# Performance work log

Hardware: AMD Instinct MI355X
Metric: run time of the kernel (lower is better)

Reference implementation:

```python
import jax, jax.numpy as jnp
from jax import lax
import numpy as np

D_MODEL, N_STATES, N_GROUPS, K_CONV = 1024, 16, 8, 4
BATCH, LENGTH = 2, 2048


def setup_inputs() -> dict:
    key = jax.random.key(0)
    ks = jax.random.split(key, 8)
    x = jax.random.normal(ks[0], (BATCH, LENGTH, D_MODEL), dtype=jnp.float32)
    in_proj_w = jax.random.normal(ks[1], (2 * D_MODEL, D_MODEL), dtype=jnp.float32) * 0.02
    in_proj_b = jnp.zeros((2 * D_MODEL,), dtype=jnp.float32)
    delta_proj_w = jax.random.uniform(ks[2], (D_MODEL, D_MODEL), dtype=jnp.float32, minval=0.001, maxval=0.1)
    a_log = jnp.log(jnp.tile(jnp.arange(1, N_STATES + 1, dtype=jnp.float32), (D_MODEL, 1)))
    b_proj_w = jax.random.normal(ks[3], (N_GROUPS * N_STATES, D_MODEL), dtype=jnp.float32) * 1e-4
    b_proj_b = jnp.zeros((N_GROUPS * N_STATES,), dtype=jnp.float32)
    c_param = jax.random.normal(ks[4], (D_MODEL, N_STATES), dtype=jnp.float32) * 0.02
    # depthwise conv (groups = d_model): kernel [D, 1, K]
    conv_w = jax.random.normal(ks[5], (D_MODEL, 1, K_CONV), dtype=jnp.float32) * (1.0 / np.sqrt(K_CONV))
    conv_b = jnp.zeros((D_MODEL,), dtype=jnp.float32)
    return {"x": x, "in_proj_w": in_proj_w, "in_proj_b": in_proj_b,
            "delta_proj_w": delta_proj_w, "a_log": a_log,
            "b_proj_w": b_proj_w, "b_proj_b": b_proj_b, "c_param": c_param,
            "conv_w": conv_w, "conv_b": conv_b}


def _causal_conv(u, conv_w, conv_b):
    # u: [B, L, D] -> depthwise causal conv along L
    D = u.shape[-1]
    K = conv_w.shape[-1]
    uc = jnp.transpose(u, (0, 2, 1))  # [B, D, L]
    uc = lax.conv_general_dilated(uc, conv_w, window_strides=(1,),
                                  padding=[(K - 1, 0)], feature_group_count=D,
                                  dimension_numbers=("NCH", "OIH", "NCH"))
    uc = uc + conv_b[None, :, None]
    return jnp.transpose(uc, (0, 2, 1))  # [B, L, D]


def _selective_scan(delta, A, Bmat, c_param, u):
    # delta,u: [B,L,D]; A: [D,N]; Bmat: [B,L,G,N]; c_param: [D,N]
    Bsz, L, D = delta.shape
    N = A.shape[1]
    G = Bmat.shape[2]
    Bexp = jnp.repeat(Bmat, D // G, axis=2)            # [B,L,D,N]
    dA = jnp.exp(delta[..., None] * A)                  # [B,L,D,N]
    dBu = (delta * u)[..., None] * Bexp                 # [B,L,D,N]

    def step(h, xs):
        da, dbu = xs
        h = da * h + dbu                                # [B,D,N]
        y = jnp.einsum("bdn,dn->bd", h, c_param)
        return h, y

    h0 = jnp.zeros((Bsz, D, N), dtype=delta.dtype)
    _, ys = lax.scan(step, h0, (jnp.moveaxis(dA, 1, 0), jnp.moveaxis(dBu, 1, 0)))
    return jnp.moveaxis(ys, 0, 1)                       # [B,L,D]


def reference(x, in_proj_w, in_proj_b, delta_proj_w, a_log, b_proj_w, b_proj_b, c_param, conv_w, conv_b):
    Bsz, L, _ = x.shape
    N = a_log.shape[1]
    G = b_proj_w.shape[0] // N
    xp = x @ in_proj_w.T + in_proj_b                    # [B,L,2D]
    u, v = jnp.split(xp, 2, axis=-1)
    delta = jax.nn.softplus(u @ delta_proj_w.T)         # [B,L,D]
    A = -jnp.exp(a_log)                                 # [D,N]
    Bmat = (u @ b_proj_w.T + b_proj_b).reshape(Bsz, L, G, N)
    u_conv = jax.nn.silu(_causal_conv(u, conv_w, conv_b))
    y = _selective_scan(delta, A, Bmat, c_param, u_conv)
    return y * jax.nn.silu(v)
```

## Files before the change

### kernel.cpp

```cpp
#include <hip/hip_runtime.h>
#include <math.h>

#define LTOT 2048
#define MROWS 4096
#define CHK 64
#define NCH (LTOT / CHK)
#define SPAD 20

typedef short bf16x8 __attribute__((ext_vector_type(8)));
typedef float f32x4  __attribute__((ext_vector_type(4)));

__device__ __forceinline__ unsigned short bf16_rne(float f) {
  unsigned u = __float_as_uint(f);
  u += 0x7FFF + ((u >> 16) & 1);
  return (unsigned short)(u >> 16);
}
__device__ __forceinline__ float bf16_to_f(unsigned short h) {
  return __uint_as_float(((unsigned)h) << 16);
}
__device__ __forceinline__ float softplus_f(float x) {
  return (x > 15.f) ? x : log1pf(expf(x));
}
__device__ __forceinline__ float silu_f(float x) {
  return x / (1.f + expf(-x));
}

__global__ __launch_bounds__(256) void k_prep(
    const float* __restrict__ x, const float* __restrict__ w1,
    const float* __restrict__ dw, const float* __restrict__ bw,
    const float* __restrict__ b1, const float* __restrict__ bb,
    unsigned short* __restrict__ xh, unsigned short* __restrict__ wfh,
    unsigned short* __restrict__ wdbAh, unsigned short* __restrict__ wdbAl,
    unsigned short* __restrict__ w1th, unsigned short* __restrict__ w1tl,
    float* __restrict__ bfull) {
  __shared__ float ts[64][65];
  const int blk = blockIdx.x;
  const int t = threadIdx.x;

  if (blk < 6144) {
    const float* src; unsigned short* h; int i;
    if (blk < 4096) { src = x;  h = xh;  i = blk * 256 + t; }
    else            { src = w1; h = wfh; i = (blk - 4096) * 256 + t; }
    const float4 v = ((const float4*)src)[i];
    ushort4 hh;
    hh.x = bf16_rne(v.x); hh.y = bf16_rne(v.y);
    hh.z = bf16_rne(v.z); hh.w = bf16_rne(v.w);
    ((ushort4*)h)[i] = hh;
  } else if (blk < 7296) {
    const float* src; unsigned short *h, *l; int i;
    if (blk < 7168) { src = dw; h = wdbAh; l = wdbAl; i = (blk - 6144) * 256 + t; }
    else            { src = bw; h = wdbAh + (size_t)1024*1024; l = wdbAl + (size_t)1024*1024;
                      i = (blk - 7168) * 256 + t; }
    const float4 v = ((const float4*)src)[i];
    ushort4 hh, ll;
    hh.x = bf16_rne(v.x); ll.x = bf16_rne(v.x - bf16_to_f(hh.x));
    hh.y = bf16_rne(v.y); ll.y = bf16_rne(v.y - bf16_to_f(hh.y));
    hh.z = bf16_rne(v.z); ll.z = bf16_rne(v.z - bf16_to_f(hh.z));
    hh.w = bf16_rne(v.w); ll.w = bf16_rne(v.w - bf16_to_f(hh.w));
    ((ushort4*)h)[i] = hh;
    ((ushort4*)l)[i] = ll;
  } else if (blk < 7552) {
    const int s = blk - 7296;
    const int k0 = (s & 15) * 64, j0 = (s >> 4) * 64;
    const int r = t >> 4, c4 = (t & 15) * 4;
    #pragma unroll
    for (int p = 0; p < 4; ++p) {
      const int row = p * 16 + r;
      const float4 v = *(const float4*)&w1[(size_t)(j0 + row) * 1024 + k0 + c4];
      ts[row][c4] = v.x; ts[row][c4+1] = v.y; ts[row][c4+2] = v.z; ts[row][c4+3] = v.w;
    }
    __syncthreads();
    #pragma unroll
    for (int p = 0; p < 4; ++p) {
      const int rk = p * 16 + r;
      ushort4 hh, ll;
      float f;
      f = ts[c4+0][rk]; hh.x = bf16_rne(f); ll.x = bf16_rne(f - bf16_to_f(hh.x));
      f = ts[c4+1][rk]; hh.y = bf16_rne(f); ll.y = bf16_rne(f - bf16_to_f(hh.y));
      f = ts[c4+2][rk]; hh.z = bf16_rne(f); ll.z = bf16_rne(f - bf16_to_f(hh.z));
      f = ts[c4+3][rk]; hh.w = bf16_rne(f); ll.w = bf16_rne(f - bf16_to_f(hh.w));
      *(ushort4*)&w1th[(size_t)(k0 + rk) * 1024 + j0 + c4] = hh;
      *(ushort4*)&w1tl[(size_t)(k0 + rk) * 1024 + j0 + c4] = ll;
    }
  } else {
    const int j = (blk - 7552) * 16 + (t >> 4);
    const int lane16 = t & 15;
    const float* W = (j < 1024) ? (dw + (size_t)j * 1024) : (bw + (size_t)(j - 1024) * 1024);
    float s = 0.f;
    for (int i = 0; i < 64; ++i) {
      const int k = lane16 + i * 16;
      s = fmaf(b1[k], W[k], s);
    }
    s += __shfl_xor(s, 8, 16);
    s += __shfl_xor(s, 4, 16);
    s += __shfl_xor(s, 2, 16);
    s += __shfl_xor(s, 1, 16);
    if (lane16 == 0) bfull[j] = s + ((j >= 1024) ? bb[j - 1024] : 0.f);
  }
}

__global__ __launch_bounds__(256) void k_wcomp2(
    const unsigned short* __restrict__ Ah_g, const unsigned short* __restrict__ Al_g,
    const unsigned short* __restrict__ Bh_g, const unsigned short* __restrict__ Bl_g,
    unsigned short* __restrict__ outh) {
  __shared__ __align__(16) unsigned short LAh[128*32];
  __shared__ __align__(16) unsigned short LAl[128*32];
  __shared__ __align__(16) unsigned short LBh[128*32];
  __shared__ __align__(16) unsigned short LBl[128*32];
  const int t = threadIdx.x;
  const int wave = t >> 6, lane = t & 63;
  const int m0 = blockIdx.y * 128;
  const int n0 = blockIdx.x * 128;
  const int wr = wave >> 1, wc = wave & 1;
  const int ln = lane & 15, kq = lane >> 4;
  const int srow = lane >> 2, scol = (lane & 3) * 8;

  f32x4 acc[4][4];
  #pragma unroll
  for (int i = 0; i < 4; ++i)
    #pragma unroll
    for (int j = 0; j < 4; ++j) acc[i][j] = (f32x4){0.f, 0.f, 0.f, 0.f};

  const unsigned short* pAh = Ah_g + (size_t)m0 * 1024;
  const unsigned short* pAl = Al_g + (size_t)m0 * 1024;
  const unsigned short* pBh = Bh_g + (size_t)n0 * 1024;
  const unsigned short* pBl = Bl_g + (size_t)n0 * 1024;

  auto stage = [&](const unsigned short* g, unsigned short* lds, int k0) {
    #pragma unroll
    for (int r = 0; r < 2; ++r) {
      const unsigned short* gp = g + (size_t)(r * 64 + wave * 16 + srow) * 1024 + k0 + scol;
      unsigned short* lp = lds + (r * 64 + wave * 16) * 32;
      __builtin_amdgcn_global_load_lds((const __attribute__((address_space(1))) void*)gp,
                                       (__attribute__((address_space(3))) void*)lp, 16, 0, 0);
    }
  };

  for (int k0 = 0; k0 < 1024; k0 += 32) {
    __syncthreads();
    stage(pAh, LAh, k0);
    stage(pAl, LAl, k0);
    stage(pBh, LBh, k0);
    stage(pBl, LBl, k0);
    __syncthreads();
    bf16x8 ah[4], al[4], bh[4], bl[4];
    #pragma unroll
    for (int i = 0; i < 4; ++i) {
      const int ar = (wr * 64 + i * 16 + ln) * 32 + kq * 8;
      const int br = (wc * 64 + i * 16 + ln) * 32 + kq * 8;
      ah[i] = *(const bf16x8*)&LAh[ar];
      al[i] = *(const bf16x8*)&LAl[ar];
      bh[i] = *(const bf16x8*)&LBh[br];
      bl[i] = *(const bf16x8*)&LBl[br];
    }
    #pragma unroll
    for (int i = 0; i < 4; ++i)
      #pragma unroll
      for (int j = 0; j < 4; ++j) {
        acc[i][j] = __builtin_amdgcn_mfma_f32_16x16x32_bf16(ah[i], bh[j], acc[i][j], 0, 0, 0);
        acc[i][j] = __builtin_amdgcn_mfma_f32_16x16x32_bf16(ah[i], bl[j], acc[i][j], 0, 0, 0);
        acc[i][j] = __builtin_amdgcn_mfma_f32_16x16x32_bf16(al[i], bh[j], acc[i][j], 0, 0, 0);
      }
  }

  const int rbase = (blockIdx.y < 8) ? 2176 : 1024;
  #pragma unroll
  for (int nj = 0; nj < 4; ++nj) {
    const int kcol = n0 + wc * 64 + nj * 16 + ln;
    #pragma unroll
    for (int mi = 0; mi < 4; ++mi) {
      const int i = m0 + wr * 64 + mi * 16 + kq * 4;
      #pragma unroll
      for (int j = 0; j < 4; ++j)
        outh[(size_t)(rbase + i + j) * 1024 + kcol] = bf16_rne(acc[mi][nj][j]);
    }
  }
}

__global__ __launch_bounds__(256) void k_mm_u(
    const unsigned short* __restrict__ xh, const unsigned short* __restrict__ wfh,
    const float* __restrict__ b1, const float* __restrict__ bfull,
    float* __restrict__ u_, float* __restrict__ v_,
    float* __restrict__ delta, float* __restrict__ Bm) {
  __shared__ __align__(16) unsigned short LAh[128*64];
  __shared__ __align__(16) unsigned short LBh[128*64];
  const int t = threadIdx.x;
  const int wave = t >> 6, lane = t & 63;
  const int flat = blockIdx.x;
  const int wg = (flat & 7) * 100 + (flat >> 3);
  const int tn = wg % 25;
  const int m0 = (wg / 25) * 128;
  const int wr = wave >> 1, wc = wave & 1;
  const int ln = lane & 15, kq = lane >> 4;
  const int srow = lane >> 3;
  const int scb  = ((lane & 7) ^ (lane >> 3)) * 8;

  f32x4 acc[4][4];
  #pragma unroll
  for (int i = 0; i < 4; ++i)
    #pragma unroll
    for (int j = 0; j < 4; ++j) acc[i][j] = (f32x4){0.f, 0.f, 0.f, 0.f};

  const unsigned short* pAh = xh + (size_t)m0 * 1024;
  const unsigned short* pBh = wfh + (size_t)(tn * 128) * 1024;

  auto stage = [&](const unsigned short* g, unsigned short* lds, int k0) {
    #pragma unroll
    for (int r = 0; r < 4; ++r) {
      const int rowb = wave * 32 + r * 8;
      const unsigned short* gp = g + (size_t)(rowb + srow) * 1024 + k0 + scb;
      unsigned short* lp = lds + rowb * 64;
      __builtin_amdgcn_global_load_lds((const __attribute__((address_space(1))) void*)gp,
                                       (__attribute__((address_space(3))) void*)lp, 16, 0, 0);
    }
  };

  for (int k0 = 0; k0 < 1024; k0 += 64) {
    __syncthreads();
    stage(pAh, LAh, k0);
    stage(pBh, LBh, k0);
    __syncthreads();
    #pragma unroll
    for (int kh = 0; kh < 2; ++kh) {
      bf16x8 ah[4], bh[4];
      #pragma unroll
      for (int i = 0; i < 4; ++i) {
        const int arow = wr * 64 + i * 16 + ln;
        const int brow = wc * 64 + i * 16 + ln;
        const int ablk = ((kh * 4 + kq) ^ (arow & 7)) * 8;
        const int bblk = ((kh * 4 + kq) ^ (brow & 7)) * 8;
        ah[i] = *(const bf16x8*)&LAh[arow * 64 + ablk];
        bh[i] = *(const bf16x8*)&LBh[brow * 64 + bblk];
      }
      #pragma unroll
      for (int i = 0; i < 4; ++i)
        #pragma unroll
        for (int j = 0; j < 4; ++j)
          acc[i][j] = __builtin_amdgcn_mfma_f32_16x16x32_bf16(ah[i], bh[j], acc[i][j], 0, 0, 0);
    }
  }

  #pragma unroll
  for (int nj = 0; nj < 4; ++nj) {
    const int colg = tn * 128 + wc * 64 + nj * 16 + ln;
    float bv;
    if (colg < 2048)      bv = b1[colg];
    else if (colg < 2176) bv = bfull[1024 + colg - 2048];
    else                  bv = bfull[colg - 2176];
    #pragma unroll
    for (int mi = 0; mi < 4; ++mi) {
      const int row = m0 + wr * 64 + mi * 16 + kq * 4;
      #pragma unroll
      for (int j = 0; j < 4; ++j) {
        const float val = acc[mi][nj][j] + bv;
        if (tn < 8)        u_[(size_t)(row + j) * 1024 + colg] = val;
        else if (tn < 16)  v_[(size_t)(row + j) * 1024 + colg - 1024] = val;
        else if (tn == 16) Bm[(size_t)(row + j) * 128 + colg - 2048] = val;
        else               delta[(size_t)(row + j) * 1024 + colg - 2176] = softplus_f(val);
      }
    }
  }
}

__global__ __launch_bounds__(256) void k_scanA(
    const float* __restrict__ delta, const float* __restrict__ u_,
    const float* __restrict__ Bm, const float* __restrict__ a_log,
    const float* __restrict__ cw, const float* __restrict__ cb,
    float* __restrict__ hend, float* __restrict__ Pp)
{
  __shared__ float sru[68][SPAD];
  __shared__ float sd[CHK][SPAD];
  __shared__ float sb[CHK][SPAD];
  __shared__ float suc[CHK][SPAD];
  const int t = threadIdx.x;
  const int bid = blockIdx.x;
  const int dblk = bid & 63;
  const int ch   = (bid >> 6) & (NCH - 1);
  const int b    = bid >> 11;
  const int d0 = dblk * 16;
  const int g  = dblk >> 3;
  const int l0 = ch * CHK;
  const size_t mb = (size_t)b * LTOT;

  {
    const int lrow = t >> 2;
    const int lc4  = (t & 3) * 4;
    const size_t r = mb + l0 + lrow;
    float4 rd = *(const float4*)&delta[r*1024 + d0 + lc4];
    float4 rb = *(const float4*)&Bm[r*128 + g*16 + lc4];
    *(float4*)&sd[lrow][lc4] = rd;
    *(float4*)&sb[lrow][lc4] = rb;
    const int sl = l0 + lrow - 4;
    float4 ru = (sl >= 0) ? *(const float4*)&u_[(mb + sl)*1024 + d0 + lc4]
                          : (float4){0.f, 0.f, 0.f, 0.f};
    *(float4*)&sru[lrow][lc4] = ru;
    if (t < 16) {
      const int rr2 = 64 + (t >> 2);
      const int sl2 = l0 + rr2 - 4;
      float4 r2 = *(const float4*)&u_[(mb + sl2)*1024 + d0 + (t & 3) * 4];
      *(float4*)&sru[rr2][(t & 3) * 4] = r2;
    }
  }
  __syncthreads();
  {
    const int c = t & 15;
    const int rb4 = (t >> 4) * 4;
    const float4 cwf = *(const float4*)&cw[(d0 + c) * 4];
    const float cbf = cb[d0 + c];
    #pragma unroll
    for (int q = 0; q < 4; ++q) {
      const int l = rb4 + q;
      float a = cbf;
      a = fmaf(sru[l+1][c], cwf.x, a);
      a = fmaf(sru[l+2][c], cwf.y, a);
      a = fmaf(sru[l+3][c], cwf.z, a);
      a = fmaf(sru[l+4][c], cwf.w, a);
      suc[l][c] = silu_f(a);
    }
  }
  __syncthreads();

  const int gi = t >> 4;
  const int n  = t & 15;
  const int d  = d0 + gi;
  const float A2 = -expf(a_log[d*16 + n]) * 1.4426950408889634f;

  float h = 0.f, P = 1.f;
  #pragma unroll 8
  for (int l = 0; l < CHK; ++l) {
    const float dv = sd[l][gi];
    const float uv = suc[l][gi];
    const float bv = sb[l][n];
    const float da = exp2f(dv * A2);
    P *= da;
    h = fmaf(da, h, dv * uv * bv);
  }
  const size_t idx = ((size_t)(b*NCH + ch) * 1024 + d) * 16 + n;
  hend[idx] = h;
  Pp[idx]   = P;
}

__global__ void k_scanB(float* hP, const float* __restrict__ Pp)
{
  const int t = blockIdx.x * 256 + threadIdx.x;
  const int b  = t >> 14;
  const int dn = t & 16383;
  float H = 0.f;
  for (int ch = 0; ch < NCH; ++ch) {
    const size_t idx = ((size_t)(b*NCH + ch) << 14) + dn;
    const float he = hP[idx];
    const float P  = Pp[idx];
    hP[idx] = H;
    H = fmaf(P, H, he);
  }
}

__global__ __launch_bounds__(256) void k_scanC(
    const float* __restrict__ v_, const float* __restrict__ delta,
    const float* __restrict__ u_, const float* __restrict__ Bm,
    const float* __restrict__ a_log, const float* __restrict__ cp,
    const float* __restrict__ cw, const float* __restrict__ cb,
    const float* __restrict__ Hstart, float* __restrict__ out)
{
  __shared__ float sru[68][SPAD];
  __shared__ float sd[CHK][SPAD];
  __shared__ float sb[CHK][SPAD];
  __shared__ float suc[CHK][SPAD];
  __shared__ float sv[CHK][SPAD];
  __shared__ float sy[CHK][SPAD];
  const int t = threadIdx.x;
  const int bid = blockIdx.x;
  const int dblk = bid & 63;
  const int ch   = (bid >> 6) & (NCH - 1);
  const int b    = bid >> 11;
  const int d0 = dblk * 16;
  const int g  = dblk >> 3;
  const int l0 = ch * CHK;
  const size_t mb = (size_t)b * LTOT;

  {
    const int lrow = t >> 2;
    const int lc4  = (t & 3) * 4;
    const size_t r = mb + l0 + lrow;
    float4 rd = *(const float4*)&delta[r*1024 + d0 + lc4];
    float4 rb = *(const float4*)&Bm[r*128 + g*16 + lc4];
    float4 rv = *(const float4*)&v_[r*1024 + d0 + lc4];
    *(float4*)&sd[lrow][lc4] = rd;
    *(float4*)&sb[lrow][lc4] = rb;
    *(float4*)&sv[lrow][lc4] = rv;
    const int sl = l0 + lrow - 4;
    float4 ru = (sl >= 0) ? *(const float4*)&u_[(mb + sl)*1024 + d0 + lc4]
                          : (float4){0.f, 0.f, 0.f, 0.f};
    *(float4*)&sru[lrow][lc4] = ru;
    if (t < 16) {
      const int rr2 = 64 + (t >> 2);
      const int sl2 = l0 + rr2 - 4;
      float4 r2 = *(const float4*)&u_[(mb + sl2)*1024 + d0 + (t & 3) * 4];
      *(float4*)&sru[rr2][(t & 3) * 4] = r2;
    }
  }
  __syncthreads();
  {
    const int c = t & 15;
    const int rb4 = (t >> 4) * 4;
    const float4 cwf = *(const float4*)&cw[(d0 + c) * 4];
    const float cbf = cb[d0 + c];
    #pragma unroll
    for (int q = 0; q < 4; ++q) {
      const int l = rb4 + q;
      float a = cbf;
      a = fmaf(sru[l+1][c], cwf.x, a);
      a = fmaf(sru[l+2][c], cwf.y, a);
      a = fmaf(sru[l+3][c], cwf.z, a);
      a = fmaf(sru[l+4][c], cwf.w, a);
      suc[l][c] = silu_f(a);
    }
  }
  __syncthreads();

  const int gi = t >> 4;
  const int n  = t & 15;
  const int d  = d0 + gi;
  const float A2 = -expf(a_log[d*16 + n]) * 1.4426950408889634f;
  const float cc = cp[d*16 + n];
  float h = Hstart[((size_t)(b*NCH + ch) * 1024 + d) * 16 + n];

  #pragma unroll
  for (int l16 = 0; l16 < CHK; l16 += 16) {
    float p[16];
    #pragma unroll
    for (int j = 0; j < 16; ++j) {
      const int l = l16 + j;
      const float dv = sd[l][gi];
      const float uv = suc[l][gi];
      const float bv = sb[l][n];
      const float da = exp2f(dv * A2);
      h = fmaf(da, h, dv * uv * bv);
      p[j] = h * cc;
    }
    float q8[8];
    #pragma unroll
    for (int j = 0; j < 8; ++j) {
      const float send = (n & 8) ? p[j]     : p[j + 8];
      const float keep = (n & 8) ? p[j + 8] : p[j];
      q8[j] = keep + __shfl_xor(send, 8, 16);
    }
    float q4[4];
    #pragma unroll
    for (int j = 0; j < 4; ++j) {
      const float send = (n & 4) ? q8[j]     : q8[j + 4];
      const float keep = (n & 4) ? q8[j + 4] : q8[j];
      q4[j] = keep + __shfl_xor(send, 4, 16);
    }
    float q2[2];
    #pragma unroll
    for (int j = 0; j < 2; ++j) {
      const float send = (n & 2) ? q4[j]     : q4[j + 2];
      const float keep = (n & 2) ? q4[j + 2] : q4[j];
      q2[j] = keep + __shfl_xor(send, 2, 16);
    }
    {
      const float send = (n & 1) ? q2[0] : q2[1];
      const float keep = (n & 1) ? q2[1] : q2[0];
      sy[l16 + n][gi] = keep + __shfl_xor(send, 1, 16);
    }
  }

  __syncthreads();
  const int rr = t >> 4;
  const int c  = t & 15;
  #pragma unroll
  for (int k = 0; k < 4; ++k) {
    const int r = rr + k * 16;
    const float vv = sv[r][c];
    out[(mb + l0 + r) * 1024 + d0 + c] = sy[r][c] * silu_f(vv);
  }
}

extern "C" void kernel_launch(void* const* d_in, const int* in_sizes, int n_in,
                              void* d_out, int out_size, void* d_ws, size_t ws_size,
                              hipStream_t stream) {
  const float* x    = (const float*)d_in[0];
  const float* w1   = (const float*)d_in[1];
  const float* b1   = (const float*)d_in[2];
  const float* dw   = (const float*)d_in[3];
  const float* alog = (const float*)d_in[4];
  const float* bw   = (const float*)d_in[5];
  const float* bb   = (const float*)d_in[6];
  const float* cp   = (const float*)d_in[7];
  const float* cw   = (const float*)d_in[8];
  const float* cb   = (const float*)d_in[9];
  float* out = (float*)d_out;

  const size_t M4 = (size_t)MROWS * 1024;
  float* u_    = (float*)d_ws;
  float* v_    = u_ + M4;
  float* delta = v_ + M4;
  float* Bm    = delta + M4;
  unsigned short* xh  = (unsigned short*)(Bm + (size_t)MROWS * 128);
  unsigned short* xl  = xh + M4;
  unsigned short* wfh = xl + M4;
  unsigned short* wfl = wfh + (size_t)3200 * 1024;
  float* bfull = (float*)(wfl + (size_t)3200 * 1024);
  unsigned short* wdbAh = (unsigned short*)delta;
  unsigned short* wdbAl = wdbAh + (size_t)1152 * 1024;
  unsigned short* w1th  = wdbAl + (size_t)1152 * 1024;
  unsigned short* w1tl  = w1th + (size_t)1024 * 1024;
  float* hend = (float*)wfh;
  float* Pp   = hend + (size_t)2 * NCH * 1024 * 16;

  k_prep<<<7624, 256, 0, stream>>>(x, w1, dw, bw, b1, bb,
                                   xh, wfh, wdbAh, wdbAl, w1th, w1tl, bfull);
  k_wcomp2<<<dim3(8, 9), 256, 0, stream>>>(wdbAh, wdbAl, w1th, w1tl, wfh);
  k_mm_u<<<800, 256, 0, stream>>>(xh, wfh, b1, bfull, u_, v_, delta, Bm);
  k_scanA<<<2 * NCH * 64, 256, 0, stream>>>(delta, u_, Bm, alog, cw, cb, hend, Pp);
  k_scanB<<<128, 256, 0, stream>>>(hend, Pp);
  k_scanC<<<2 * NCH * 64, 256, 0, stream>>>(v_, delta, u_, Bm, alog, cp, cw, cb, hend, out);
}
```

Baseline: 205.2 us.

## Double-buffer LDS tiles in input projection GEMM to overlap loads with MFMA

Converts the k_mm_u GEMM main loop from single-buffered LDS staging to a double-buffered ping-pong scheme. The next K-tile's global-to-LDS loads are issued before computing on the current tile, with explicit vmcnt waits and raw s_barrier calls replacing __syncthreads. This is meant to hide global load latency behind MFMA work. In exchange it doubles the LDS footprint, which may reduce occupancy, and it depends on hand-tuned waitcnt counts being correct.

```diff
diff --git a/kernel.cpp b/kernel.cpp
--- a/kernel.cpp
+++ b/kernel.cpp
@@ -182,8 +182,8 @@
     const float* __restrict__ b1, const float* __restrict__ bfull,
     float* __restrict__ u_, float* __restrict__ v_,
     float* __restrict__ delta, float* __restrict__ Bm) {
-  __shared__ __align__(16) unsigned short LAh[128*64];
-  __shared__ __align__(16) unsigned short LBh[128*64];
+  __shared__ __align__(16) unsigned short LA[2][128*64];
+  __shared__ __align__(16) unsigned short LB[2][128*64];
   const int t = threadIdx.x;
   const int wave = t >> 6, lane = t & 63;
   const int flat = blockIdx.x;
@@ -215,11 +215,23 @@
     }
   };
 
-  for (int k0 = 0; k0 < 1024; k0 += 64) {
-    __syncthreads();
-    stage(pAh, LAh, k0);
-    stage(pBh, LBh, k0);
-    __syncthreads();
+  stage(pAh, LA[0], 0);
+  stage(pBh, LB[0], 0);
+
+  for (int tt = 0; tt < 16; ++tt) {
+    const int cur = tt & 1;
+    if (tt < 15) {
+      stage(pAh, LA[cur ^ 1], (tt + 1) * 64);
+      stage(pBh, LB[cur ^ 1], (tt + 1) * 64);
+      asm volatile("s_waitcnt vmcnt(8)" ::: "memory");
+    } else {
+      asm volatile("s_waitcnt vmcnt(0)" ::: "memory");
+    }
+    __builtin_amdgcn_s_barrier();
+    __builtin_amdgcn_sched_barrier(0);
+
+    const unsigned short* la = LA[cur];
+    const unsigned short* lb = LB[cur];
     #pragma unroll
     for (int kh = 0; kh < 2; ++kh) {
       bf16x8 ah[4], bh[4];
@@ -229,14 +241,19 @@
         const int brow = wc * 64 + i * 16 + ln;
         const int ablk = ((kh * 4 + kq) ^ (arow & 7)) * 8;
         const int bblk = ((kh * 4 + kq) ^ (brow & 7)) * 8;
-        ah[i] = *(const bf16x8*)&LAh[arow * 64 + ablk];
-        bh[i] = *(const bf16x8*)&LBh[brow * 64 + bblk];
+        ah[i] = *(const bf16x8*)&la[arow * 64 + ablk];
+        bh[i] = *(const bf16x8*)&lb[brow * 64 + bblk];
       }
       #pragma unroll
       for (int i = 0; i < 4; ++i)
         #pragma unroll
         for (int j = 0; j < 4; ++j)
           acc[i][j] = __builtin_amdgcn_mfma_f32_16x16x32_bf16(ah[i], bh[j], acc[i][j], 0, 0, 0);
+    }
+
+    if (tt < 15) {
+      __builtin_amdgcn_sched_barrier(0);
+      __builtin_amdgcn_s_barrier();
     }
   }
 
```

Result: faster. 201.2 us (-2.0%).
